# Kernel tuning notes

Measured on AMD Instinct MI355X. Metric: run time of the kernel, lower is better.

## Reference

```python
import jax, jax.numpy as jnp
import numpy as np


def _transmittance(delta_density):
    # exclusive cumulative sum along the sample axis, then exp(-.)
    csum = jnp.cumsum(delta_density[..., :-1, :], axis=-2)
    zeros = jnp.zeros((*csum.shape[:-2], 1, csum.shape[-1]), dtype=delta_density.dtype)
    return jnp.exp(-jnp.concatenate([zeros, csum], axis=-2))


def setup_inputs() -> dict:
    key = jax.random.key(0)
    ks = jax.random.split(key, 6)
    R, S = 16384, 256
    return {
        "object_rgbs": jax.random.uniform(ks[0], (R, S, 3), dtype=jnp.float32),
        "medium_rgbs": jax.random.uniform(ks[1], (R, S, 3), dtype=jnp.float32),
        "direct_coeffs": jax.random.uniform(ks[2], (R, S, 3), dtype=jnp.float32),
        "backscatter_coeffs": jax.random.uniform(ks[3], (R, S, 3), dtype=jnp.float32),
        "densities": jax.random.uniform(ks[4], (R, S, 1), dtype=jnp.float32),
        "deltas": jax.random.uniform(ks[5], (R, S, 1), dtype=jnp.float32) * 0.05,
    }


def reference(object_rgbs, medium_rgbs, direct_coeffs, backscatter_coeffs, densities, deltas):
    object_rgbs = jnp.nan_to_num(object_rgbs)
    medium_rgbs = jnp.nan_to_num(medium_rgbs)
    direct_coeffs = jnp.nan_to_num(direct_coeffs)
    backscatter_coeffs = jnp.nan_to_num(backscatter_coeffs)

    deltas = jax.lax.stop_gradient(deltas)  # ray_samples.deltas.detach()
    delta_densities = deltas * densities                       # [R,S,1]

    object_transmittance = _transmittance(delta_densities)     # [R,S,1]
    object_alphas = 1.0 - jnp.exp(-delta_densities)            # [R,S,1]
    object_weights = object_transmittance * object_alphas      # [R,S,1]

    restored = jnp.clip(jnp.sum(object_weights * object_rgbs, axis=-2), 0.0, 1.0)

    direct_attenuation = _transmittance(direct_coeffs * deltas)             # [R,S,3]
    direct_weights = object_transmittance * direct_attenuation * object_alphas
    direct_ray = jnp.sum(direct_weights * object_rgbs, axis=-2)             # [R,3]
    direct = jnp.clip(direct_ray, 0.0, 1.0)

    bs_dd = backscatter_coeffs * deltas                                     # [R,S,3]
    backscattering = _transmittance(bs_dd)
    medium_alphas = 1.0 - jnp.exp(-bs_dd)
    backscatter_weights = object_transmittance * backscattering * medium_alphas
    backscatter_ray = jnp.sum(backscatter_weights * medium_rgbs, axis=-2)   # [R,3]
    backscatter = jnp.clip(backscatter_ray, 0.0, 1.0)

    rgb = jnp.clip(direct_ray + backscatter_ray, 0.0, 1.0)
    object_mask = jnp.clip(jnp.sum(object_weights, axis=-2), 0.0, 1.0)

    return (rgb, restored, direct, backscatter, object_transmittance,
            object_alphas, object_weights, direct_coeffs[:, 0, :],
            backscatter_coeffs[:, 0, :], object_mask)
```

## Files before the change

kernel.cpp:

```cpp
#include <hip/hip_runtime.h>


__device__ __forceinline__ float clip01(float x) {
    return fminf(fmaxf(x, 0.0f), 1.0f);
}

__device__ __forceinline__ float wave_exscan(float v, int lane) {
    float x = v;
#pragma unroll
    for (int off = 1; off < 64; off <<= 1) {
        float y = __shfl_up(x, off, 64);
        x += (lane >= off) ? y : 0.0f;
    }
    return x - v;
}

__device__ __forceinline__ float wave_sum(float v) {
#pragma unroll
    for (int off = 32; off; off >>= 1) v += __shfl_xor(v, off, 64);
    return v;
}

__global__ __launch_bounds__(256, 2) void seathru_render(
    const float* __restrict__ g_orgb,
    const float* __restrict__ g_mrgb,
    const float* __restrict__ g_dc,
    const float* __restrict__ g_bc,
    const float* __restrict__ g_den,
    const float* __restrict__ g_del,
    float* __restrict__ out, int R)
{
    const int S = 256;
    const int ray  = blockIdx.x * 4 + (threadIdx.x >> 6);
    const int lane = threadIdx.x & 63;
    if (ray >= R) return;

    const size_t b3 = (size_t)ray * (S * 3);
    const size_t b1 = (size_t)ray * S;
    const size_t RS = (size_t)R * S;

    float4 dl4 = *((const float4*)(g_del + b1) + lane);
    float4 dn4 = *((const float4*)(g_den + b1) + lane);

    float dcv[12], orv[12], bcv[12], mrv[12];
    {
        const float4* p = (const float4*)(g_dc + b3) + lane * 3;
        *(float4*)&dcv[0] = p[0]; *(float4*)&dcv[4] = p[1]; *(float4*)&dcv[8] = p[2];
    }
    {
        const float4* p = (const float4*)(g_orgb + b3) + lane * 3;
        *(float4*)&orv[0] = p[0]; *(float4*)&orv[4] = p[1]; *(float4*)&orv[8] = p[2];
    }
    {
        const float4* p = (const float4*)(g_bc + b3) + lane * 3;
        *(float4*)&bcv[0] = p[0]; *(float4*)&bcv[4] = p[1]; *(float4*)&bcv[8] = p[2];
    }
    {
        const float4* p = (const float4*)(g_mrgb + b3) + lane * 3;
        *(float4*)&mrv[0] = p[0]; *(float4*)&mrv[4] = p[1]; *(float4*)&mrv[8] = p[2];
    }

    float del[4] = {dl4.x, dl4.y, dl4.z, dl4.w};
    float den[4] = {dn4.x, dn4.y, dn4.z, dn4.w};

    float dd[4], ex_dd[4];
    float run = 0.0f;
#pragma unroll
    for (int i = 0; i < 4; ++i) { dd[i] = del[i] * den[i]; ex_dd[i] = run; run += dd[i]; }
    const float off_dd = wave_exscan(run, lane);

    float T[4], alpha[4], w[4];
#pragma unroll
    for (int i = 0; i < 4; ++i) {
        T[i]     = __expf(-(off_dd + ex_dd[i]));
        alpha[i] = 1.0f - __expf(-dd[i]);
        w[i]     = T[i] * alpha[i];
    }

    float* outT = out + (size_t)12 * R;
    float* outA = outT + RS;
    float* outW = outA + RS;
    {
        float4 t4 = {T[0], T[1], T[2], T[3]};
        float4 a4 = {alpha[0], alpha[1], alpha[2], alpha[3]};
        float4 w4 = {w[0], w[1], w[2], w[3]};
        *((float4*)(outT + b1) + lane) = t4;
        *((float4*)(outA + b1) + lane) = a4;
        *((float4*)(outW + b1) + lane) = w4;
    }

    float acc_dir[3], acc_bs[3], acc_rest[3];
    float acc_mask = w[0] + w[1] + w[2] + w[3];

#pragma unroll
    for (int c = 0; c < 3; ++c) {
        float dcd[4], exd[4], rund = 0.0f;
#pragma unroll
        for (int i = 0; i < 4; ++i) { dcd[i] = dcv[i * 3 + c] * del[i]; exd[i] = rund; rund += dcd[i]; }
        const float offd = wave_exscan(rund, lane);

        float ad = 0.0f, ar = 0.0f;
#pragma unroll
        for (int i = 0; i < 4; ++i) {
            const float da = __expf(-(offd + exd[i]));
            const float o  = orv[i * 3 + c];
            ad += T[i] * da * alpha[i] * o;
            ar += w[i] * o;
        }
        acc_dir[c] = ad;
        acc_rest[c] = ar;

        float bsd[4], exb[4], runb = 0.0f;
#pragma unroll
        for (int i = 0; i < 4; ++i) { bsd[i] = bcv[i * 3 + c] * del[i]; exb[i] = runb; runb += bsd[i]; }
        const float offb = wave_exscan(runb, lane);

        float ab = 0.0f;
#pragma unroll
        for (int i = 0; i < 4; ++i) {
            const float B  = __expf(-(offb + exb[i]));
            const float ma = 1.0f - __expf(-bsd[i]);
            ab += T[i] * B * ma * mrv[i * 3 + c];
        }
        acc_bs[c] = ab;
    }

#pragma unroll
    for (int c = 0; c < 3; ++c) {
        acc_dir[c]  = wave_sum(acc_dir[c]);
        acc_bs[c]   = wave_sum(acc_bs[c]);
        acc_rest[c] = wave_sum(acc_rest[c]);
    }
    acc_mask = wave_sum(acc_mask);

    if (lane == 0) {
        float* rgb  = out;
        float* rest = out + (size_t)3 * R;
        float* dir  = out + (size_t)6 * R;
        float* bs   = out + (size_t)9 * R;
        float* dc0  = out + (size_t)12 * R + 3 * RS;
        float* bc0  = dc0 + (size_t)3 * R;
        float* mask = bc0 + (size_t)3 * R;
#pragma unroll
        for (int c = 0; c < 3; ++c) {
            const float d = acc_dir[c], b = acc_bs[c];
            rgb[ray * 3 + c]  = clip01(d + b);
            rest[ray * 3 + c] = clip01(acc_rest[c]);
            dir[ray * 3 + c]  = clip01(d);
            bs[ray * 3 + c]   = clip01(b);
            dc0[ray * 3 + c]  = dcv[c];
            bc0[ray * 3 + c]  = bcv[c];
        }
        mask[ray] = clip01(acc_mask);
    }
}

extern "C" void kernel_launch(void* const* d_in, const int* in_sizes, int n_in,
                              void* d_out, int out_size, void* d_ws, size_t ws_size,
                              hipStream_t stream) {
    const float* orgb = (const float*)d_in[0];
    const float* mrgb = (const float*)d_in[1];
    const float* dc   = (const float*)d_in[2];
    const float* bc   = (const float*)d_in[3];
    const float* den  = (const float*)d_in[4];
    const float* del  = (const float*)d_in[5];

    const int S = 256;
    const int R = in_sizes[0] / (S * 3);

    dim3 block(256);
    dim3 grid((R + 3) / 4);
    seathru_render<<<grid, block, 0, stream>>>(orgb, mrgb, dc, bc, den, del,
                                               (float*)d_out, R);
}
```

Before: 240.5 us.

## Map one ray per block and fuse all seven scans with combined exponents

Restructures the kernel so each 256-thread block handles one ray with one sample per thread. The transmittance products are folded into the scan values as summed exponents, so seven prefix scans run together in one shuffle loop, combined across waves through shared memory. Exponentials switch to exp2f with log2e pre-scaling. This removes the serialized per-channel wave scans and the large register arrays, at the cost of block-level syncs and less aligned 12-byte loads.

```diff
diff --git a/kernel.cpp b/kernel.cpp
--- a/kernel.cpp
+++ b/kernel.cpp
@@ -1,27 +1,15 @@
 #include <hip/hip_runtime.h>
 
+
+#define LOG2E 1.4426950408889634f
+
+struct F3 { float x, y, z; };
 
 __device__ __forceinline__ float clip01(float x) {
     return fminf(fmaxf(x, 0.0f), 1.0f);
 }
 
-__device__ __forceinline__ float wave_exscan(float v, int lane) {
-    float x = v;
-#pragma unroll
-    for (int off = 1; off < 64; off <<= 1) {
-        float y = __shfl_up(x, off, 64);
-        x += (lane >= off) ? y : 0.0f;
-    }
-    return x - v;
-}
-
-__device__ __forceinline__ float wave_sum(float v) {
-#pragma unroll
-    for (int off = 32; off; off >>= 1) v += __shfl_xor(v, off, 64);
-    return v;
-}
-
-__global__ __launch_bounds__(256, 2) void seathru_render(
+__global__ __launch_bounds__(256, 4) void seathru_render(
     const float* __restrict__ g_orgb,
     const float* __restrict__ g_mrgb,
     const float* __restrict__ g_dc,
@@ -31,109 +19,104 @@
     float* __restrict__ out, int R)
 {
     const int S = 256;
-    const int ray  = blockIdx.x * 4 + (threadIdx.x >> 6);
-    const int lane = threadIdx.x & 63;
-    if (ray >= R) return;
+    const int ray  = blockIdx.x;
+    const int tid  = threadIdx.x;
+    const int lane = tid & 63;
+    const int wv   = tid >> 6;
 
-    const size_t b3 = (size_t)ray * (S * 3);
-    const size_t b1 = (size_t)ray * S;
+    const size_t b1 = (size_t)ray * S + tid;
+    const size_t b3 = b1 * 3;
     const size_t RS = (size_t)R * S;
 
-    float4 dl4 = *((const float4*)(g_del + b1) + lane);
-    float4 dn4 = *((const float4*)(g_den + b1) + lane);
+    const float del = g_del[b1] * LOG2E;
+    const float den = g_den[b1];
+    const F3 dc  = *((const F3*)(g_dc   + b3));
+    const F3 bc  = *((const F3*)(g_bc   + b3));
+    const F3 orv = *((const F3*)(g_orgb + b3));
+    const F3 mr  = *((const F3*)(g_mrgb + b3));
 
-    float dcv[12], orv[12], bcv[12], mrv[12];
-    {
-        const float4* p = (const float4*)(g_dc + b3) + lane * 3;
-        *(float4*)&dcv[0] = p[0]; *(float4*)&dcv[4] = p[1]; *(float4*)&dcv[8] = p[2];
-    }
-    {
-        const float4* p = (const float4*)(g_orgb + b3) + lane * 3;
-        *(float4*)&orv[0] = p[0]; *(float4*)&orv[4] = p[1]; *(float4*)&orv[8] = p[2];
-    }
-    {
-        const float4* p = (const float4*)(g_bc + b3) + lane * 3;
-        *(float4*)&bcv[0] = p[0]; *(float4*)&bcv[4] = p[1]; *(float4*)&bcv[8] = p[2];
-    }
-    {
-        const float4* p = (const float4*)(g_mrgb + b3) + lane * 3;
-        *(float4*)&mrv[0] = p[0]; *(float4*)&mrv[4] = p[1]; *(float4*)&mrv[8] = p[2];
+    const float dd   = del * den;
+    const float bsd0 = bc.x * del, bsd1 = bc.y * del, bsd2 = bc.z * del;
+    float own[7];
+    own[0] = dd;
+    own[1] = dd + dc.x * del;
+    own[2] = dd + dc.y * del;
+    own[3] = dd + dc.z * del;
+    own[4] = dd + bsd0;
+    own[5] = dd + bsd1;
+    own[6] = dd + bsd2;
+
+    float v[7];
+#pragma unroll
+    for (int j = 0; j < 7; ++j) v[j] = own[j];
+#pragma unroll
+    for (int off = 1; off < 64; off <<= 1) {
+        float y[7];
+#pragma unroll
+        for (int j = 0; j < 7; ++j) y[j] = __shfl_up(v[j], off, 64);
+#pragma unroll
+        for (int j = 0; j < 7; ++j) v[j] += (lane >= off) ? y[j] : 0.0f;
     }
 
-    float del[4] = {dl4.x, dl4.y, dl4.z, dl4.w};
-    float den[4] = {dn4.x, dn4.y, dn4.z, dn4.w};
+    __shared__ float s_tot[4][8];
+    __shared__ float s_red[4][10];
+    if (lane == 63) {
+#pragma unroll
+        for (int j = 0; j < 7; ++j) s_tot[wv][j] = v[j];
+    }
+    __syncthreads();
 
-    float dd[4], ex_dd[4];
-    float run = 0.0f;
+    float ex[7];
 #pragma unroll
-    for (int i = 0; i < 4; ++i) { dd[i] = del[i] * den[i]; ex_dd[i] = run; run += dd[i]; }
-    const float off_dd = wave_exscan(run, lane);
+    for (int j = 0; j < 7; ++j) ex[j] = v[j] - own[j];
+#pragma unroll
+    for (int w2 = 0; w2 < 3; ++w2) {
+        if (wv > w2) {
+#pragma unroll
+            for (int j = 0; j < 7; ++j) ex[j] += s_tot[w2][j];
+        }
+    }
 
-    float T[4], alpha[4], w[4];
-#pragma unroll
-    for (int i = 0; i < 4; ++i) {
-        T[i]     = __expf(-(off_dd + ex_dd[i]));
-        alpha[i] = 1.0f - __expf(-dd[i]);
-        w[i]     = T[i] * alpha[i];
-    }
+    const float T     = exp2f(-ex[0]);
+    const float alpha = 1.0f - exp2f(-dd);
+    const float w     = T * alpha;
 
     float* outT = out + (size_t)12 * R;
     float* outA = outT + RS;
     float* outW = outA + RS;
-    {
-        float4 t4 = {T[0], T[1], T[2], T[3]};
-        float4 a4 = {alpha[0], alpha[1], alpha[2], alpha[3]};
-        float4 w4 = {w[0], w[1], w[2], w[3]};
-        *((float4*)(outT + b1) + lane) = t4;
-        *((float4*)(outA + b1) + lane) = a4;
-        *((float4*)(outW + b1) + lane) = w4;
-    }
+    outT[b1] = T;
+    outA[b1] = alpha;
+    outW[b1] = w;
 
-    float acc_dir[3], acc_bs[3], acc_rest[3];
-    float acc_mask = w[0] + w[1] + w[2] + w[3];
+    float a[10];
+    a[0] = exp2f(-ex[1]) * alpha * orv.x;
+    a[1] = exp2f(-ex[2]) * alpha * orv.y;
+    a[2] = exp2f(-ex[3]) * alpha * orv.z;
+    a[3] = exp2f(-ex[4]) * (1.0f - exp2f(-bsd0)) * mr.x;
+    a[4] = exp2f(-ex[5]) * (1.0f - exp2f(-bsd1)) * mr.y;
+    a[5] = exp2f(-ex[6]) * (1.0f - exp2f(-bsd2)) * mr.z;
+    a[6] = w * orv.x;
+    a[7] = w * orv.y;
+    a[8] = w * orv.z;
+    a[9] = w;
 
 #pragma unroll
-    for (int c = 0; c < 3; ++c) {
-        float dcd[4], exd[4], rund = 0.0f;
+    for (int off = 32; off; off >>= 1) {
 #pragma unroll
-        for (int i = 0; i < 4; ++i) { dcd[i] = dcv[i * 3 + c] * del[i]; exd[i] = rund; rund += dcd[i]; }
-        const float offd = wave_exscan(rund, lane);
+        for (int j = 0; j < 10; ++j) a[j] += __shfl_xor(a[j], off, 64);
+    }
+    if (lane == 0) {
+#pragma unroll
+        for (int j = 0; j < 10; ++j) s_red[wv][j] = a[j];
+    }
+    __syncthreads();
 
-        float ad = 0.0f, ar = 0.0f;
+    if (tid == 0) {
+        float t[10];
 #pragma unroll
-        for (int i = 0; i < 4; ++i) {
-            const float da = __expf(-(offd + exd[i]));
-            const float o  = orv[i * 3 + c];
-            ad += T[i] * da * alpha[i] * o;
-            ar += w[i] * o;
-        }
-        acc_dir[c] = ad;
-        acc_rest[c] = ar;
+        for (int j = 0; j < 10; ++j)
+            t[j] = s_red[0][j] + s_red[1][j] + s_red[2][j] + s_red[3][j];
 
-        float bsd[4], exb[4], runb = 0.0f;
-#pragma unroll
-        for (int i = 0; i < 4; ++i) { bsd[i] = bcv[i * 3 + c] * del[i]; exb[i] = runb; runb += bsd[i]; }
-        const float offb = wave_exscan(runb, lane);
-
-        float ab = 0.0f;
-#pragma unroll
-        for (int i = 0; i < 4; ++i) {
-            const float B  = __expf(-(offb + exb[i]));
-            const float ma = 1.0f - __expf(-bsd[i]);
-            ab += T[i] * B * ma * mrv[i * 3 + c];
-        }
-        acc_bs[c] = ab;
-    }
-
-#pragma unroll
-    for (int c = 0; c < 3; ++c) {
-        acc_dir[c]  = wave_sum(acc_dir[c]);
-        acc_bs[c]   = wave_sum(acc_bs[c]);
-        acc_rest[c] = wave_sum(acc_rest[c]);
-    }
-    acc_mask = wave_sum(acc_mask);
-
-    if (lane == 0) {
         float* rgb  = out;
         float* rest = out + (size_t)3 * R;
         float* dir  = out + (size_t)6 * R;
@@ -141,17 +124,26 @@
         float* dc0  = out + (size_t)12 * R + 3 * RS;
         float* bc0  = dc0 + (size_t)3 * R;
         float* mask = bc0 + (size_t)3 * R;
-#pragma unroll
-        for (int c = 0; c < 3; ++c) {
-            const float d = acc_dir[c], b = acc_bs[c];
-            rgb[ray * 3 + c]  = clip01(d + b);
-            rest[ray * 3 + c] = clip01(acc_rest[c]);
-            dir[ray * 3 + c]  = clip01(d);
-            bs[ray * 3 + c]   = clip01(b);
-            dc0[ray * 3 + c]  = dcv[c];
-            bc0[ray * 3 + c]  = bcv[c];
-        }
-        mask[ray] = clip01(acc_mask);
+
+        rgb[ray * 3 + 0]  = clip01(t[0] + t[3]);
+        rgb[ray * 3 + 1]  = clip01(t[1] + t[4]);
+        rgb[ray * 3 + 2]  = clip01(t[2] + t[5]);
+        dir[ray * 3 + 0]  = clip01(t[0]);
+        dir[ray * 3 + 1]  = clip01(t[1]);
+        dir[ray * 3 + 2]  = clip01(t[2]);
+        bs[ray * 3 + 0]   = clip01(t[3]);
+        bs[ray * 3 + 1]   = clip01(t[4]);
+        bs[ray * 3 + 2]   = clip01(t[5]);
+        rest[ray * 3 + 0] = clip01(t[6]);
+        rest[ray * 3 + 1] = clip01(t[7]);
+        rest[ray * 3 + 2] = clip01(t[8]);
+        dc0[ray * 3 + 0]  = dc.x;
+        dc0[ray * 3 + 1]  = dc.y;
+        dc0[ray * 3 + 2]  = dc.z;
+        bc0[ray * 3 + 0]  = bc.x;
+        bc0[ray * 3 + 1]  = bc.y;
+        bc0[ray * 3 + 2]  = bc.z;
+        mask[ray]         = clip01(t[9]);
     }
 }
 
@@ -169,7 +161,7 @@
     const int R = in_sizes[0] / (S * 3);
 
     dim3 block(256);
-    dim3 grid((R + 3) / 4);
+    dim3 grid(R);
     seathru_render<<<grid, block, 0, stream>>>(orgb, mrgb, dc, bc, den, del,
                                                (float*)d_out, R);
 }
```

Result: slower. 245.8 us (+2.2%).

## Fold transmittance products into combined scans and use DPP wave scans

Applied to the files above, without the earlier changes.

Each ray's products T*D and T*B are rewritten as a single exponential of a combined prefix sum, giving seven scans computed together. Those scans and the final reductions use batched DPP row operations instead of shuffle loops, and exponentials are switched to exp2 with the deltas prescaled by log2(e). Fewer exp calls and cheaper cross-lane operations are meant to cut ALU and LDS-shuffle latency, and the occupancy hint is raised to four. Folding the sums together changes floating-point rounding slightly, and the higher occupancy hint may cause register spills.

```diff
diff --git a/kernel.cpp b/kernel.cpp
--- a/kernel.cpp
+++ b/kernel.cpp
@@ -1,27 +1,35 @@
 #include <hip/hip_runtime.h>
 
+
+#define LOG2E 1.4426950408889634f
 
 __device__ __forceinline__ float clip01(float x) {
     return fminf(fmaxf(x, 0.0f), 1.0f);
 }
 
-__device__ __forceinline__ float wave_exscan(float v, int lane) {
-    float x = v;
-#pragma unroll
-    for (int off = 1; off < 64; off <<= 1) {
-        float y = __shfl_up(x, off, 64);
-        x += (lane >= off) ? y : 0.0f;
-    }
-    return x - v;
+template <int CTRL, int ROW_MASK, bool BND>
+__device__ __forceinline__ float dpp_mov(float v) {
+    return __int_as_float(__builtin_amdgcn_update_dpp(
+        0, __float_as_int(v), CTRL, ROW_MASK, 0xf, BND));
 }
 
-__device__ __forceinline__ float wave_sum(float v) {
+template <int N>
+__device__ __forceinline__ void wave_iscan(float (&v)[N]) {
 #pragma unroll
-    for (int off = 32; off; off >>= 1) v += __shfl_xor(v, off, 64);
-    return v;
+    for (int j = 0; j < N; ++j) v[j] += dpp_mov<0x111, 0xf, true>(v[j]);
+#pragma unroll
+    for (int j = 0; j < N; ++j) v[j] += dpp_mov<0x112, 0xf, true>(v[j]);
+#pragma unroll
+    for (int j = 0; j < N; ++j) v[j] += dpp_mov<0x114, 0xf, true>(v[j]);
+#pragma unroll
+    for (int j = 0; j < N; ++j) v[j] += dpp_mov<0x118, 0xf, true>(v[j]);
+#pragma unroll
+    for (int j = 0; j < N; ++j) v[j] += dpp_mov<0x142, 0xa, false>(v[j]);
+#pragma unroll
+    for (int j = 0; j < N; ++j) v[j] += dpp_mov<0x143, 0xc, false>(v[j]);
 }
 
-__global__ __launch_bounds__(256, 2) void seathru_render(
+__global__ __launch_bounds__(256, 4) void seathru_render(
     const float* __restrict__ g_orgb,
     const float* __restrict__ g_mrgb,
     const float* __restrict__ g_dc,
@@ -42,39 +50,73 @@
     float4 dl4 = *((const float4*)(g_del + b1) + lane);
     float4 dn4 = *((const float4*)(g_den + b1) + lane);
 
-    float dcv[12], orv[12], bcv[12], mrv[12];
+    float dcv[12], bcv[12], orv[12], mrv[12];
     {
         const float4* p = (const float4*)(g_dc + b3) + lane * 3;
         *(float4*)&dcv[0] = p[0]; *(float4*)&dcv[4] = p[1]; *(float4*)&dcv[8] = p[2];
+    }
+    {
+        const float4* p = (const float4*)(g_bc + b3) + lane * 3;
+        *(float4*)&bcv[0] = p[0]; *(float4*)&bcv[4] = p[1]; *(float4*)&bcv[8] = p[2];
     }
     {
         const float4* p = (const float4*)(g_orgb + b3) + lane * 3;
         *(float4*)&orv[0] = p[0]; *(float4*)&orv[4] = p[1]; *(float4*)&orv[8] = p[2];
     }
     {
-        const float4* p = (const float4*)(g_bc + b3) + lane * 3;
-        *(float4*)&bcv[0] = p[0]; *(float4*)&bcv[4] = p[1]; *(float4*)&bcv[8] = p[2];
-    }
-    {
         const float4* p = (const float4*)(g_mrgb + b3) + lane * 3;
         *(float4*)&mrv[0] = p[0]; *(float4*)&mrv[4] = p[1]; *(float4*)&mrv[8] = p[2];
     }
 
-    float del[4] = {dl4.x, dl4.y, dl4.z, dl4.w};
-    float den[4] = {dn4.x, dn4.y, dn4.z, dn4.w};
+    const float del[4] = {dl4.x * LOG2E, dl4.y * LOG2E, dl4.z * LOG2E, dl4.w * LOG2E};
+    const float den[4] = {dn4.x, dn4.y, dn4.z, dn4.w};
 
-    float dd[4], ex_dd[4];
-    float run = 0.0f;
-#pragma unroll
-    for (int i = 0; i < 4; ++i) { dd[i] = del[i] * den[i]; ex_dd[i] = run; run += dd[i]; }
-    const float off_dd = wave_exscan(run, lane);
-
-    float T[4], alpha[4], w[4];
+    float dd[4], alpha[4];
 #pragma unroll
     for (int i = 0; i < 4; ++i) {
-        T[i]     = __expf(-(off_dd + ex_dd[i]));
-        alpha[i] = 1.0f - __expf(-dd[i]);
-        w[i]     = T[i] * alpha[i];
+        dd[i]    = del[i] * den[i];
+        alpha[i] = 1.0f - exp2f(-dd[i]);
+    }
+
+    float aorv[12];
+    float mamr[12];
+#pragma unroll
+    for (int i = 0; i < 4; ++i) {
+#pragma unroll
+        for (int c = 0; c < 3; ++c) {
+            aorv[i * 3 + c] = alpha[i] * orv[i * 3 + c];
+            const float bsd = bcv[i * 3 + c] * del[i];
+            mamr[i * 3 + c] = (1.0f - exp2f(-bsd)) * mrv[i * 3 + c];
+        }
+    }
+
+    float ser[7][4];
+    float run[7];
+#pragma unroll
+    for (int q = 0; q < 7; ++q) run[q] = 0.0f;
+#pragma unroll
+    for (int i = 0; i < 4; ++i) {
+        ser[0][i] = run[0]; run[0] += dd[i];
+#pragma unroll
+        for (int c = 0; c < 3; ++c) {
+            ser[1 + c][i] = run[1 + c]; run[1 + c] += dd[i] + dcv[i * 3 + c] * del[i];
+            ser[4 + c][i] = run[4 + c]; run[4 + c] += dd[i] + bcv[i * 3 + c] * del[i];
+        }
+    }
+
+    float sc[7];
+#pragma unroll
+    for (int q = 0; q < 7; ++q) sc[q] = run[q];
+    wave_iscan<7>(sc);
+    float off[7];
+#pragma unroll
+    for (int q = 0; q < 7; ++q) off[q] = sc[q] - run[q];
+
+    float T[4], w[4];
+#pragma unroll
+    for (int i = 0; i < 4; ++i) {
+        T[i] = exp2f(-(off[0] + ser[0][i]));
+        w[i] = T[i] * alpha[i];
     }
 
     float* outT = out + (size_t)12 * R;
@@ -89,51 +131,25 @@
         *((float4*)(outW + b1) + lane) = w4;
     }
 
-    float acc_dir[3], acc_bs[3], acc_rest[3];
-    float acc_mask = w[0] + w[1] + w[2] + w[3];
-
+    float acc[10];
 #pragma unroll
     for (int c = 0; c < 3; ++c) {
-        float dcd[4], exd[4], rund = 0.0f;
-#pragma unroll
-        for (int i = 0; i < 4; ++i) { dcd[i] = dcv[i * 3 + c] * del[i]; exd[i] = rund; rund += dcd[i]; }
-        const float offd = wave_exscan(rund, lane);
-
-        float ad = 0.0f, ar = 0.0f;
+        float ad = 0.0f, ab = 0.0f, ar = 0.0f;
 #pragma unroll
         for (int i = 0; i < 4; ++i) {
-            const float da = __expf(-(offd + exd[i]));
-            const float o  = orv[i * 3 + c];
-            ad += T[i] * da * alpha[i] * o;
-            ar += w[i] * o;
+            ad += exp2f(-(off[1 + c] + ser[1 + c][i])) * aorv[i * 3 + c];
+            ab += exp2f(-(off[4 + c] + ser[4 + c][i])) * mamr[i * 3 + c];
+            ar += T[i] * aorv[i * 3 + c];
         }
-        acc_dir[c] = ad;
-        acc_rest[c] = ar;
+        acc[c]     = ad;
+        acc[3 + c] = ab;
+        acc[6 + c] = ar;
+    }
+    acc[9] = w[0] + w[1] + w[2] + w[3];
 
-        float bsd[4], exb[4], runb = 0.0f;
-#pragma unroll
-        for (int i = 0; i < 4; ++i) { bsd[i] = bcv[i * 3 + c] * del[i]; exb[i] = runb; runb += bsd[i]; }
-        const float offb = wave_exscan(runb, lane);
+    wave_iscan<10>(acc);
 
-        float ab = 0.0f;
-#pragma unroll
-        for (int i = 0; i < 4; ++i) {
-            const float B  = __expf(-(offb + exb[i]));
-            const float ma = 1.0f - __expf(-bsd[i]);
-            ab += T[i] * B * ma * mrv[i * 3 + c];
-        }
-        acc_bs[c] = ab;
-    }
-
-#pragma unroll
-    for (int c = 0; c < 3; ++c) {
-        acc_dir[c]  = wave_sum(acc_dir[c]);
-        acc_bs[c]   = wave_sum(acc_bs[c]);
-        acc_rest[c] = wave_sum(acc_rest[c]);
-    }
-    acc_mask = wave_sum(acc_mask);
-
-    if (lane == 0) {
+    if (lane == 63) {
         float* rgb  = out;
         float* rest = out + (size_t)3 * R;
         float* dir  = out + (size_t)6 * R;
@@ -143,15 +159,22 @@
         float* mask = bc0 + (size_t)3 * R;
 #pragma unroll
         for (int c = 0; c < 3; ++c) {
-            const float d = acc_dir[c], b = acc_bs[c];
+            const float d = acc[c], b = acc[3 + c];
             rgb[ray * 3 + c]  = clip01(d + b);
-            rest[ray * 3 + c] = clip01(acc_rest[c]);
             dir[ray * 3 + c]  = clip01(d);
             bs[ray * 3 + c]   = clip01(b);
-            dc0[ray * 3 + c]  = dcv[c];
-            bc0[ray * 3 + c]  = bcv[c];
+            rest[ray * 3 + c] = clip01(acc[6 + c]);
         }
-        mask[ray] = clip01(acc_mask);
+        mask[ray] = clip01(acc[9]);
+    }
+    if (lane == 0) {
+        float* dc0 = out + (size_t)12 * R + 3 * RS;
+        float* bc0 = dc0 + (size_t)3 * R;
+#pragma unroll
+        for (int c = 0; c < 3; ++c) {
+            dc0[ray * 3 + c] = dcv[c];
+            bc0[ray * 3 + c] = bcv[c];
+        }
     }
 }
 
```

Result: no change. 239.6 us (-0.4%).
